# Kernel tuning notes

Hardware: AMD Instinct MI355X
Metric: run time of the kernel (lower is better)

Reference implementation:

```python
import jax, jax.numpy as jnp
import numpy as np

N_NODES = 50000

def _gat_layer(x, src, dst, W, a_l, a_r, bias, alpha, agg, act, n_nodes):
    # x: [N, in]; W: [in, H*F]; a_l, a_r: [H, F]; bias: [H*F]
    H, F = a_l.shape
    z = (x @ W).reshape(n_nodes, H, F)                      # [N,H,F]
    el = jnp.einsum('nhf,hf->nh', z, a_l)                   # [N,H]
    er = jnp.einsum('nhf,hf->nh', z, a_r)                   # [N,H]
    e = jax.nn.leaky_relu(el[src] + er[dst], alpha)         # [E,H]
    # segment softmax over in-edges of each destination node
    m = jax.ops.segment_max(e, dst, num_segments=n_nodes)   # [N,H]
    ex = jnp.exp(e - m[dst])                                # [E,H]
    s = jax.ops.segment_sum(ex, dst, num_segments=n_nodes)  # [N,H]
    attn = ex / jnp.maximum(s[dst], 1e-9)                   # [E,H]
    msg = attn[:, :, None] * z[src]                         # [E,H,F]
    h = jax.ops.segment_sum(msg, dst, num_segments=n_nodes) # [N,H,F]
    # identity residual (in_feats == H*F) as in DGL GATConv
    h = h + x.reshape(n_nodes, -1, F)
    h = h + bias.reshape(1, H, F)
    if agg == 'flatten':
        h = h.reshape(n_nodes, H * F)
    else:  # mean over heads
        h = h.mean(axis=1)
    if act is not None:
        h = act(h)
    return h


def setup_inputs() -> dict:
    key = jax.random.key(0)
    ks = jax.random.split(key, 14)
    N, E, D = N_NODES, 800000, 128
    H, F = 4, 32
    sc_in = 1.0 / np.sqrt(D)
    sc_h = 1.0 / np.sqrt(H * F)
    inp = {
        'feats': jax.random.normal(ks[0], (N, D), jnp.float32),
        'src': jax.random.randint(ks[1], (E,), 0, N),
        'dst': jax.random.randint(ks[2], (E,), 0, N),
        'W1': jax.random.normal(ks[3], (D, H * F), jnp.float32) * sc_in,
        'al1': jax.random.normal(ks[4], (H, F), jnp.float32) * sc_h,
        'ar1': jax.random.normal(ks[5], (H, F), jnp.float32) * sc_h,
        'b1': jnp.zeros((H * F,), jnp.float32),
        'W2': jax.random.normal(ks[6], (H * F, H * F), jnp.float32) * sc_h,
        'al2': jax.random.normal(ks[7], (H, F), jnp.float32) * sc_h,
        'ar2': jax.random.normal(ks[8], (H, F), jnp.float32) * sc_h,
        'b2': jnp.zeros((H * F,), jnp.float32),
        'Wp': jax.random.normal(ks[9], (F, 1), jnp.float32) / np.sqrt(F),
        'bp': jnp.zeros((1,), jnp.float32),
    }
    return inp


def reference(feats, src, dst, W1, al1, ar1, b1, W2, al2, ar2, b2, Wp, bp):
    h = _gat_layer(feats, src, dst, W1, al1, ar1, b1, 0.2, 'flatten', jax.nn.elu, N_NODES)
    h = _gat_layer(h, src, dst, W2, al2, ar2, b2, 0.2, 'mean', None, N_NODES)
    return h @ Wp + bp  # [N, 1]
```

## Files before the change

kernel.cpp:

```cpp
#include <hip/hip_runtime.h>
#include <hip/hip_bf16.h>

#define NN 50000
#define NE 800000
#define HF 128

#define OFF_FLAG   0u
#define OFF_ROWPTR 256u
#define OFF_BSUM   200272u
#define OFF_BOFF   200480u
#define OFF_DEG    200704u
#define OFF_FILL   400896u
#define OFF_ADJ    601088u
#define OFF_FX     3801088u
#define OFF_WC1    16601088u
#define OFF_WC2    16633856u
#define OFF_PAR    16666624u
#define OFF_Z      16668672u
#define OFF_H1     29468672u
#define OFF_EL     42268672u
#define OFF_ER     43068672u

typedef __hip_bfloat16 bf16;
typedef unsigned short us16;

#define N_SMALL 33569

typedef __attribute__((ext_vector_type(8))) short bf16x8;
typedef __attribute__((ext_vector_type(4))) float f32x4;

__device__ __forceinline__ float us2f(us16 u) {
  union { unsigned int i; float f; } c; c.i = ((unsigned int)u) << 16; return c.f;
}
__device__ __forceinline__ us16 f2us(float f) {
  bf16 h = __float2bfloat16(f);
  union { bf16 h; us16 u; } c; c.h = h; return c.u;
}
__device__ __forceinline__ float blo(unsigned v) {
  union { unsigned i; float f; } c; c.i = v << 16; return c.f;
}
__device__ __forceinline__ float bhi(unsigned v) {
  union { unsigned i; float f; } c; c.i = v & 0xffff0000u; return c.f;
}
__device__ __forceinline__ unsigned pk2(float a, float b) {
  return (unsigned)f2us(a) | ((unsigned)f2us(b) << 16);
}

__global__ __launch_bounds__(64) void k_detect(const void* __restrict__ w1raw,
                                               int* __restrict__ flag) {
  const us16* u = (const us16*)w1raw;
  int lane = threadIdx.x;
  int mx = 0;
  for (int i = lane; i < 2048; i += 64) {
    int e = (u[i] >> 7) & 0xFF;
    mx = mx > e ? mx : e;
  }
#pragma unroll
  for (int m = 32; m >= 1; m >>= 1) {
    int o = __shfl_xor(mx, m);
    mx = mx > o ? mx : o;
  }
  if (lane == 0) *flag = (mx >= 135) ? 1 : 0;
}

__global__ __launch_bounds__(256) void k_canon_feats(const void* __restrict__ src,
                                                     us16* __restrict__ dst,
                                                     const int* __restrict__ flag) {
  int i = (blockIdx.x * 256 + threadIdx.x) * 4;
  if (i >= NN * HF) return;
  if (*flag) {
    float4 v = *(const float4*)((const float*)src + i);
    ushort4 o;
    o.x = f2us(v.x); o.y = f2us(v.y); o.z = f2us(v.z); o.w = f2us(v.w);
    *(ushort4*)(dst + i) = o;
  } else {
    *(ushort4*)(dst + i) = *(const ushort4*)((const us16*)src + i);
  }
}

__global__ __launch_bounds__(256) void k_canon_small(
    const void* s0, const void* s1, const void* s2, const void* s3, const void* s4,
    const void* s5, const void* s6, const void* s7, const void* s8, const void* s9,
    us16* d0, us16* d1, us16* d2, us16* d3, us16* d4,
    us16* d5, us16* d6, us16* d7, us16* d8, us16* d9,
    const int* __restrict__ flag) {
  const void* sp[10] = {s0, s1, s2, s3, s4, s5, s6, s7, s8, s9};
  us16* dp[10] = {d0, d1, d2, d3, d4, d5, d6, d7, d8, d9};
  const int cnt[10] = {16384, 16384, 128, 128, 128, 128, 128, 128, 32, 1};
  int f = *flag;
  int gid = blockIdx.x * 256 + threadIdx.x;
  int base = 0;
#pragma unroll
  for (int p = 0; p < 10; ++p) {
    int loc = gid - base;
    if (loc >= 0 && loc < cnt[p])
      dp[p][loc] = f ? f2us(((const float*)sp[p])[loc]) : ((const us16*)sp[p])[loc];
    base += cnt[p];
  }
}

__global__ void k_rank(const int* __restrict__ dst, int* __restrict__ fill,
                       int* __restrict__ rank) {
  int e = blockIdx.x * 256 + threadIdx.x;
  if (e < NE) rank[e] = atomicAdd(&fill[dst[e]], 1);
}

__global__ __launch_bounds__(1024) void k_s1(const int* __restrict__ deg,
                                             int* __restrict__ bsum) {
  __shared__ int red[1024];
  int t = threadIdx.x;
  int i = blockIdx.x * 1024 + t;
  red[t] = (i < NN) ? deg[i] : 0;
  __syncthreads();
  for (int s = 512; s > 0; s >>= 1) {
    if (t < s) red[t] += red[t + s];
    __syncthreads();
  }
  if (t == 0) bsum[blockIdx.x] = red[0];
}

__global__ __launch_bounds__(64) void k_s2(const int* __restrict__ bsum,
                                           int* __restrict__ boff,
                                           int* __restrict__ rowptr) {
  int lane = threadIdx.x;
  const int NB = (NN + 1023) / 1024;
  int v = (lane < NB) ? bsum[lane] : 0;
  int orig = v;
#pragma unroll
  for (int off = 1; off < 64; off <<= 1) {
    int u = __shfl_up(v, off);
    if (lane >= off) v += u;
  }
  if (lane < NB) boff[lane] = v - orig;
  if (lane == 0) rowptr[NN] = NE;
}

__global__ __launch_bounds__(1024) void k_s3(const int* __restrict__ deg,
                                             const int* __restrict__ boff,
                                             int* __restrict__ rowptr) {
  __shared__ int part[1024];
  int t = threadIdx.x;
  int i = blockIdx.x * 1024 + t;
  int d = (i < NN) ? deg[i] : 0;
  part[t] = d;
  __syncthreads();
  for (int off = 1; off < 1024; off <<= 1) {
    int v = (t >= off) ? part[t - off] : 0;
    __syncthreads();
    part[t] += v;
    __syncthreads();
  }
  if (i < NN) rowptr[i] = boff[blockIdx.x] + part[t] - d;
}

__global__ void k_place(const int* __restrict__ src, const int* __restrict__ dst,
                        const int* __restrict__ rowptr, const int* __restrict__ rank,
                        int* __restrict__ adj) {
  int e = blockIdx.x * 256 + threadIdx.x;
  if (e < NE) adj[rowptr[dst[e]] + rank[e]] = src[e];
}

__global__ __launch_bounds__(256) void k_gemm(const us16* __restrict__ X,
                                              const us16* __restrict__ W,
                                              us16* __restrict__ Z,
                                              const us16* __restrict__ al,
                                              const us16* __restrict__ ar,
                                              float* __restrict__ el,
                                              float* __restrict__ er) {
  __shared__ us16 Wl[HF * HF];
  int tid = threadIdx.x;
  for (int e = tid; e < HF * HF; e += 256) {
    int k = e >> 7, n = e & 127;
    int d = ((((k >> 5) * 8 + (n >> 4)) * 4 + ((k >> 3) & 3)) * 16 + (n & 15)) * 8 + (k & 7);
    Wl[d] = W[e];
  }
  __syncthreads();

  int w = tid >> 6;
  int lane = tid & 63;
  int q = lane >> 4;
  int c = lane & 15;
  int m0 = blockIdx.x * 64 + w * 16;

  int rA = m0 + c;
  if (rA >= NN) rA = NN - 1;
  const us16* xrow = X + (size_t)rA * HF;

  f32x4 acc[8] = {};
#pragma unroll
  for (int s = 0; s < 4; ++s) {
    bf16x8 a = *(const bf16x8*)&xrow[s * 32 + q * 8];
#pragma unroll
    for (int t = 0; t < 8; ++t) {
      bf16x8 b = *(const bf16x8*)&Wl[((((s * 8) + t) * 4 + q) * 16 + c) * 8];
      acc[t] = __builtin_amdgcn_mfma_f32_16x16x32_bf16(a, b, acc[t], 0, 0, 0);
    }
  }

#pragma unroll
  for (int reg = 0; reg < 4; ++reg) {
    int row = m0 + q * 4 + reg;
    if (row < NN) {
      us16* zrow = Z + (size_t)row * HF;
#pragma unroll
      for (int t = 0; t < 8; ++t) zrow[t * 16 + c] = f2us(acc[t][reg]);
    }
  }

  float alv[8], arv[8];
#pragma unroll
  for (int t = 0; t < 8; ++t) {
    alv[t] = us2f(al[t * 16 + c]);
    arv[t] = us2f(ar[t * 16 + c]);
  }
#pragma unroll
  for (int reg = 0; reg < 4; ++reg) {
    int row = m0 + q * 4 + reg;
    float pl[4], pr[4];
#pragma unroll
    for (int h = 0; h < 4; ++h) {
      pl[h] = acc[2 * h][reg] * alv[2 * h] + acc[2 * h + 1][reg] * alv[2 * h + 1];
      pr[h] = acc[2 * h][reg] * arv[2 * h] + acc[2 * h + 1][reg] * arv[2 * h + 1];
    }
#pragma unroll
    for (int m = 1; m < 16; m <<= 1) {
#pragma unroll
      for (int h = 0; h < 4; ++h) {
        pl[h] += __shfl_xor(pl[h], m);
        pr[h] += __shfl_xor(pr[h], m);
      }
    }
    if (row < NN) {
      int cc = c & 3;
      float vl = cc == 0 ? pl[0] : cc == 1 ? pl[1] : cc == 2 ? pl[2] : pl[3];
      float vr = cc == 0 ? pr[0] : cc == 1 ? pr[1] : cc == 2 ? pr[2] : pr[3];
      if (c < 4) el[row * 4 + cc] = vl;
      else if (c < 8) er[row * 4 + cc] = vr;
    }
  }
}

template <int LAYER>
__global__ __launch_bounds__(256) void k_agg(
    const us16* __restrict__ Z, const float* __restrict__ el,
    const float* __restrict__ er, const int* __restrict__ rowptr,
    const int* __restrict__ adj, const us16* __restrict__ resid,
    const us16* __restrict__ bias, us16* __restrict__ Hout,
    const us16* __restrict__ Wp, const us16* __restrict__ bp,
    void* __restrict__ out, const int* __restrict__ flag) {
  int n = blockIdx.x * 4 + (threadIdx.x >> 6);
  int lane = threadIdx.x & 63;
  int g = lane >> 4;
  int p = lane & 15;
  int hl = p >> 2;
  int f0 = p * 8;
  int begin = rowptr[n];
  int deg = rowptr[n + 1] - begin;
  float erh = er[n * 4 + hl];

  float acc[8] = {};
  float ssum = 0.f;
  int i = g;
  for (; i + 4 < deg; i += 8) {
    int s0 = adj[begin + i];
    int s1 = adj[begin + i + 4];
    float l0 = el[s0 * 4 + hl];
    float l1 = el[s1 * 4 + hl];
    uint4 za = *(const uint4*)&Z[(size_t)s0 * HF + f0];
    uint4 zb = *(const uint4*)&Z[(size_t)s1 * HF + f0];
    float sc0 = l0 + erh; sc0 = sc0 > 0.f ? sc0 : 0.2f * sc0;
    float sc1 = l1 + erh; sc1 = sc1 > 0.f ? sc1 : 0.2f * sc1;
    float ex0 = __expf(sc0);
    float ex1 = __expf(sc1);
    ssum += ex0 + ex1;
    acc[0] = fmaf(ex0, blo(za.x), acc[0]); acc[1] = fmaf(ex0, bhi(za.x), acc[1]);
    acc[2] = fmaf(ex0, blo(za.y), acc[2]); acc[3] = fmaf(ex0, bhi(za.y), acc[3]);
    acc[4] = fmaf(ex0, blo(za.z), acc[4]); acc[5] = fmaf(ex0, bhi(za.z), acc[5]);
    acc[6] = fmaf(ex0, blo(za.w), acc[6]); acc[7] = fmaf(ex0, bhi(za.w), acc[7]);
    acc[0] = fmaf(ex1, blo(zb.x), acc[0]); acc[1] = fmaf(ex1, bhi(zb.x), acc[1]);
    acc[2] = fmaf(ex1, blo(zb.y), acc[2]); acc[3] = fmaf(ex1, bhi(zb.y), acc[3]);
    acc[4] = fmaf(ex1, blo(zb.z), acc[4]); acc[5] = fmaf(ex1, bhi(zb.z), acc[5]);
    acc[6] = fmaf(ex1, blo(zb.w), acc[6]); acc[7] = fmaf(ex1, bhi(zb.w), acc[7]);
  }
  if (i < deg) {
    int s = adj[begin + i];
    float sc = el[s * 4 + hl] + erh;
    sc = sc > 0.f ? sc : 0.2f * sc;
    float ex = __expf(sc);
    ssum += ex;
    uint4 zq = *(const uint4*)&Z[(size_t)s * HF + f0];
    acc[0] = fmaf(ex, blo(zq.x), acc[0]); acc[1] = fmaf(ex, bhi(zq.x), acc[1]);
    acc[2] = fmaf(ex, blo(zq.y), acc[2]); acc[3] = fmaf(ex, bhi(zq.y), acc[3]);
    acc[4] = fmaf(ex, blo(zq.z), acc[4]); acc[5] = fmaf(ex, bhi(zq.z), acc[5]);
    acc[6] = fmaf(ex, blo(zq.w), acc[6]); acc[7] = fmaf(ex, bhi(zq.w), acc[7]);
  }
  ssum += __shfl_xor(ssum, 16); ssum += __shfl_xor(ssum, 32);
#pragma unroll
  for (int j = 0; j < 8; ++j) {
    acc[j] += __shfl_xor(acc[j], 16);
    acc[j] += __shfl_xor(acc[j], 32);
  }
  float inv = 1.f / fmaxf(ssum, 1e-9f);

  uint4 xq = *(const uint4*)&resid[(size_t)n * HF + f0];
  uint4 bq = *(const uint4*)&bias[f0];
  float t0 = fmaf(acc[0], inv, blo(xq.x) + blo(bq.x));
  float t1 = fmaf(acc[1], inv, bhi(xq.x) + bhi(bq.x));
  float t2 = fmaf(acc[2], inv, blo(xq.y) + blo(bq.y));
  float t3 = fmaf(acc[3], inv, bhi(xq.y) + bhi(bq.y));
  float t4 = fmaf(acc[4], inv, blo(xq.z) + blo(bq.z));
  float t5 = fmaf(acc[5], inv, bhi(xq.z) + bhi(bq.z));
  float t6 = fmaf(acc[6], inv, blo(xq.w) + blo(bq.w));
  float t7 = fmaf(acc[7], inv, bhi(xq.w) + bhi(bq.w));

  if (LAYER == 1) {
    t0 = t0 > 0.f ? t0 : __expf(t0) - 1.f;
    t1 = t1 > 0.f ? t1 : __expf(t1) - 1.f;
    t2 = t2 > 0.f ? t2 : __expf(t2) - 1.f;
    t3 = t3 > 0.f ? t3 : __expf(t3) - 1.f;
    t4 = t4 > 0.f ? t4 : __expf(t4) - 1.f;
    t5 = t5 > 0.f ? t5 : __expf(t5) - 1.f;
    t6 = t6 > 0.f ? t6 : __expf(t6) - 1.f;
    t7 = t7 > 0.f ? t7 : __expf(t7) - 1.f;
    if (g == 0) {
      uint4 o;
      o.x = pk2(t0, t1); o.y = pk2(t2, t3); o.z = pk2(t4, t5); o.w = pk2(t6, t7);
      *(uint4*)&Hout[(size_t)n * HF + f0] = o;
    }
  } else {
    t0 += __shfl_xor(t0, 4); t0 += __shfl_xor(t0, 8);
    t1 += __shfl_xor(t1, 4); t1 += __shfl_xor(t1, 8);
    t2 += __shfl_xor(t2, 4); t2 += __shfl_xor(t2, 8);
    t3 += __shfl_xor(t3, 4); t3 += __shfl_xor(t3, 8);
    t4 += __shfl_xor(t4, 4); t4 += __shfl_xor(t4, 8);
    t5 += __shfl_xor(t5, 4); t5 += __shfl_xor(t5, 8);
    t6 += __shfl_xor(t6, 4); t6 += __shfl_xor(t6, 8);
    t7 += __shfl_xor(t7, 4); t7 += __shfl_xor(t7, 8);
    int fw = (p & 3) * 8;
    float pr = 0.25f * (t0 * us2f(Wp[fw]) + t1 * us2f(Wp[fw + 1]) +
                        t2 * us2f(Wp[fw + 2]) + t3 * us2f(Wp[fw + 3]) +
                        t4 * us2f(Wp[fw + 4]) + t5 * us2f(Wp[fw + 5]) +
                        t6 * us2f(Wp[fw + 6]) + t7 * us2f(Wp[fw + 7]));
    pr += __shfl_xor(pr, 1); pr += __shfl_xor(pr, 2);
    if (lane == 0) {
      float res = pr + us2f(bp[0]);
      if (*flag) ((float*)out)[n] = res;
      else ((us16*)out)[n] = f2us(res);
    }
  }
}

extern "C" void kernel_launch(void* const* d_in, const int* in_sizes, int n_in,
                              void* d_out, int out_size, void* d_ws, size_t ws_size,
                              hipStream_t stream) {
  const int* src = (const int*)d_in[1];
  const int* dst = (const int*)d_in[2];
  char* ws = (char*)d_ws;
  int* flag   = (int*)(ws + OFF_FLAG);
  int* rowptr = (int*)(ws + OFF_ROWPTR);
  int* bsum   = (int*)(ws + OFF_BSUM);
  int* boff   = (int*)(ws + OFF_BOFF);
  int* fill   = (int*)(ws + OFF_FILL);
  int* adj    = (int*)(ws + OFF_ADJ);
  us16* fx    = (us16*)(ws + OFF_FX);
  us16* wc1   = (us16*)(ws + OFF_WC1);
  us16* wc2   = (us16*)(ws + OFF_WC2);
  us16* al1   = (us16*)(ws + OFF_PAR + 0);
  us16* ar1   = (us16*)(ws + OFF_PAR + 256);
  us16* b1    = (us16*)(ws + OFF_PAR + 512);
  us16* al2   = (us16*)(ws + OFF_PAR + 768);
  us16* ar2   = (us16*)(ws + OFF_PAR + 1024);
  us16* b2    = (us16*)(ws + OFF_PAR + 1280);
  us16* wp    = (us16*)(ws + OFF_PAR + 1536);
  us16* bp    = (us16*)(ws + OFF_PAR + 1792);
  us16* z     = (us16*)(ws + OFF_Z);
  us16* h1    = (us16*)(ws + OFF_H1);
  float* el   = (float*)(ws + OFF_EL);
  float* er   = (float*)(ws + OFF_ER);
  int* rank   = (int*)(ws + OFF_Z);

  const int NB = (NN + 1023) / 1024;

  hipMemsetAsync(fill, 0, OFF_ADJ - OFF_FILL, stream);

  hipLaunchKernelGGL(k_detect, dim3(1), dim3(64), 0, stream, d_in[3], flag);
  hipLaunchKernelGGL(k_canon_feats, dim3(6250), dim3(256), 0, stream, d_in[0], fx, flag);
  hipLaunchKernelGGL(k_canon_small, dim3((N_SMALL + 255) / 256), dim3(256), 0, stream,
                     d_in[3], d_in[7], d_in[4], d_in[5], d_in[6],
                     d_in[8], d_in[9], d_in[10], d_in[11], d_in[12],
                     wc1, wc2, al1, ar1, b1, al2, ar2, b2, wp, bp, flag);

  hipLaunchKernelGGL(k_rank, dim3(3125), dim3(256), 0, stream, dst, fill, rank);
  hipLaunchKernelGGL(k_s1, dim3(NB), dim3(1024), 0, stream, fill, bsum);
  hipLaunchKernelGGL(k_s2, dim3(1), dim3(64), 0, stream, bsum, boff, rowptr);
  hipLaunchKernelGGL(k_s3, dim3(NB), dim3(1024), 0, stream, fill, boff, rowptr);
  hipLaunchKernelGGL(k_place, dim3(3125), dim3(256), 0, stream, src, dst, rowptr, rank, adj);

  hipLaunchKernelGGL(k_gemm, dim3((NN + 63) / 64), dim3(256), 0, stream, fx, wc1, z,
                     al1, ar1, el, er);
  hipLaunchKernelGGL((k_agg<1>), dim3(NN / 4), dim3(256), 0, stream, z, el, er, rowptr, adj,
                     fx, b1, h1, (us16*)nullptr, (us16*)nullptr, (void*)nullptr, flag);
  hipLaunchKernelGGL(k_gemm, dim3((NN + 63) / 64), dim3(256), 0, stream, h1, wc2, z,
                     al2, ar2, el, er);
  hipLaunchKernelGGL((k_agg<2>), dim3(NN / 4), dim3(256), 0, stream, z, el, er, rowptr, adj,
                     h1, b2, (us16*)nullptr, wp, bp, d_out, flag);
}
```

Measured before the change: 264.0 us.

## Fuse detect, canonicalize and edge-rank kernels into one prep launch with padded counters

Merges the dtype detection, feature and parameter canonicalization, and the atomic in-degree ranking into a single kernel whose block ranges do different jobs. Each block recomputes the dtype flag locally, so no separate detect launch is needed. The per-node atomic counters are spread 64 bytes apart to reduce atomic contention, and they now live in the H1 buffer. This cuts four launches to one and lets the atomics overlap the conversion work, at the cost of a larger memset, redundant detection reads in every conversion block, and strided counter reads in the scans.

Result: faster. 254.5 us (-3.6%).

```diff
diff --git a/kernel.cpp b/kernel.cpp
--- a/kernel.cpp
+++ b/kernel.cpp
@@ -26,6 +26,11 @@
 
 #define N_SMALL 33569
 
+#define PREP_RANK_B   3125
+#define PREP_FEATS_B  6250
+#define PREP_SMALL_B  132
+#define PREP_GRID     (PREP_RANK_B + PREP_FEATS_B + PREP_SMALL_B)
+
 typedef __attribute__((ext_vector_type(8))) short bf16x8;
 typedef __attribute__((ext_vector_type(4))) float f32x4;
 
@@ -46,12 +51,10 @@
   return (unsigned)f2us(a) | ((unsigned)f2us(b) << 16);
 }
 
-__global__ __launch_bounds__(64) void k_detect(const void* __restrict__ w1raw,
-                                               int* __restrict__ flag) {
-  const us16* u = (const us16*)w1raw;
-  int lane = threadIdx.x;
+__device__ __forceinline__ int detect_f32(const us16* __restrict__ u) {
+  int t = threadIdx.x;
   int mx = 0;
-  for (int i = lane; i < 2048; i += 64) {
+  for (int i = t; i < 2048; i += 256) {
     int e = (u[i] >> 7) & 0xFF;
     mx = mx > e ? mx : e;
   }
@@ -60,57 +63,63 @@
     int o = __shfl_xor(mx, m);
     mx = mx > o ? mx : o;
   }
-  if (lane == 0) *flag = (mx >= 135) ? 1 : 0;
-}
-
-__global__ __launch_bounds__(256) void k_canon_feats(const void* __restrict__ src,
-                                                     us16* __restrict__ dst,
-                                                     const int* __restrict__ flag) {
-  int i = (blockIdx.x * 256 + threadIdx.x) * 4;
-  if (i >= NN * HF) return;
-  if (*flag) {
-    float4 v = *(const float4*)((const float*)src + i);
-    ushort4 o;
-    o.x = f2us(v.x); o.y = f2us(v.y); o.z = f2us(v.z); o.w = f2us(v.w);
-    *(ushort4*)(dst + i) = o;
-  } else {
-    *(ushort4*)(dst + i) = *(const ushort4*)((const us16*)src + i);
-  }
-}
-
-__global__ __launch_bounds__(256) void k_canon_small(
+  __shared__ int sred[4];
+  if ((t & 63) == 0) sred[t >> 6] = mx;
+  __syncthreads();
+  int a = sred[0] > sred[1] ? sred[0] : sred[1];
+  int b = sred[2] > sred[3] ? sred[2] : sred[3];
+  int r = a > b ? a : b;
+  return r >= 135;
+}
+
+__global__ __launch_bounds__(256) void k_prep(
+    const void* __restrict__ feats, us16* __restrict__ fx,
     const void* s0, const void* s1, const void* s2, const void* s3, const void* s4,
     const void* s5, const void* s6, const void* s7, const void* s8, const void* s9,
     us16* d0, us16* d1, us16* d2, us16* d3, us16* d4,
     us16* d5, us16* d6, us16* d7, us16* d8, us16* d9,
-    const int* __restrict__ flag) {
-  const void* sp[10] = {s0, s1, s2, s3, s4, s5, s6, s7, s8, s9};
-  us16* dp[10] = {d0, d1, d2, d3, d4, d5, d6, d7, d8, d9};
-  const int cnt[10] = {16384, 16384, 128, 128, 128, 128, 128, 128, 32, 1};
-  int f = *flag;
-  int gid = blockIdx.x * 256 + threadIdx.x;
-  int base = 0;
-#pragma unroll
-  for (int p = 0; p < 10; ++p) {
-    int loc = gid - base;
-    if (loc >= 0 && loc < cnt[p])
-      dp[p][loc] = f ? f2us(((const float*)sp[p])[loc]) : ((const us16*)sp[p])[loc];
-    base += cnt[p];
-  }
-}
-
-__global__ void k_rank(const int* __restrict__ dst, int* __restrict__ fill,
-                       int* __restrict__ rank) {
-  int e = blockIdx.x * 256 + threadIdx.x;
-  if (e < NE) rank[e] = atomicAdd(&fill[dst[e]], 1);
-}
-
-__global__ __launch_bounds__(1024) void k_s1(const int* __restrict__ deg,
+    const int* __restrict__ dst, int* __restrict__ fillp, int* __restrict__ rank,
+    int* __restrict__ flag) {
+  int b = blockIdx.x;
+  if (b < PREP_RANK_B) {
+    int e = b * 256 + threadIdx.x;
+    if (e < NE) rank[e] = atomicAdd(&fillp[dst[e] * 16], 1);
+    return;
+  }
+  int f = detect_f32((const us16*)s0);
+  if (b == PREP_RANK_B && threadIdx.x == 0) *flag = f;
+  if (b < PREP_RANK_B + PREP_FEATS_B) {
+    int i = ((b - PREP_RANK_B) * 256 + threadIdx.x) * 4;
+    if (f) {
+      float4 v = *(const float4*)((const float*)feats + i);
+      ushort4 o;
+      o.x = f2us(v.x); o.y = f2us(v.y); o.z = f2us(v.z); o.w = f2us(v.w);
+      *(ushort4*)(fx + i) = o;
+    } else {
+      *(ushort4*)(fx + i) = *(const ushort4*)((const us16*)feats + i);
+    }
+  } else {
+    const void* sp[10] = {s0, s1, s2, s3, s4, s5, s6, s7, s8, s9};
+    us16* dp[10] = {d0, d1, d2, d3, d4, d5, d6, d7, d8, d9};
+    const int cnt[10] = {16384, 16384, 128, 128, 128, 128, 128, 128, 32, 1};
+    int gid = (b - PREP_RANK_B - PREP_FEATS_B) * 256 + threadIdx.x;
+    int base = 0;
+#pragma unroll
+    for (int p = 0; p < 10; ++p) {
+      int loc = gid - base;
+      if (loc >= 0 && loc < cnt[p])
+        dp[p][loc] = f ? f2us(((const float*)sp[p])[loc]) : ((const us16*)sp[p])[loc];
+      base += cnt[p];
+    }
+  }
+}
+
+__global__ __launch_bounds__(1024) void k_s1(const int* __restrict__ fillp,
                                              int* __restrict__ bsum) {
   __shared__ int red[1024];
   int t = threadIdx.x;
   int i = blockIdx.x * 1024 + t;
-  red[t] = (i < NN) ? deg[i] : 0;
+  red[t] = (i < NN) ? fillp[i * 16] : 0;
   __syncthreads();
   for (int s = 512; s > 0; s >>= 1) {
     if (t < s) red[t] += red[t + s];
@@ -135,13 +144,13 @@
   if (lane == 0) rowptr[NN] = NE;
 }
 
-__global__ __launch_bounds__(1024) void k_s3(const int* __restrict__ deg,
+__global__ __launch_bounds__(1024) void k_s3(const int* __restrict__ fillp,
                                              const int* __restrict__ boff,
                                              int* __restrict__ rowptr) {
   __shared__ int part[1024];
   int t = threadIdx.x;
   int i = blockIdx.x * 1024 + t;
-  int d = (i < NN) ? deg[i] : 0;
+  int d = (i < NN) ? fillp[i * 16] : 0;
   part[t] = d;
   __syncthreads();
   for (int off = 1; off < 1024; off <<= 1) {
@@ -360,7 +369,6 @@
   int* rowptr = (int*)(ws + OFF_ROWPTR);
   int* bsum   = (int*)(ws + OFF_BSUM);
   int* boff   = (int*)(ws + OFF_BOFF);
-  int* fill   = (int*)(ws + OFF_FILL);
   int* adj    = (int*)(ws + OFF_ADJ);
   us16* fx    = (us16*)(ws + OFF_FX);
   us16* wc1   = (us16*)(ws + OFF_WC1);
@@ -378,22 +386,22 @@
   float* el   = (float*)(ws + OFF_EL);
   float* er   = (float*)(ws + OFF_ER);
   int* rank   = (int*)(ws + OFF_Z);
+  int* fillp  = (int*)(ws + OFF_H1);
 
   const int NB = (NN + 1023) / 1024;
 
-  hipMemsetAsync(fill, 0, OFF_ADJ - OFF_FILL, stream);
-
-  hipLaunchKernelGGL(k_detect, dim3(1), dim3(64), 0, stream, d_in[3], flag);
-  hipLaunchKernelGGL(k_canon_feats, dim3(6250), dim3(256), 0, stream, d_in[0], fx, flag);
-  hipLaunchKernelGGL(k_canon_small, dim3((N_SMALL + 255) / 256), dim3(256), 0, stream,
+  hipMemsetAsync(fillp, 0, (size_t)NN * 16 * 4, stream);
+
+  hipLaunchKernelGGL(k_prep, dim3(PREP_GRID), dim3(256), 0, stream,
+                     d_in[0], fx,
                      d_in[3], d_in[7], d_in[4], d_in[5], d_in[6],
                      d_in[8], d_in[9], d_in[10], d_in[11], d_in[12],
-                     wc1, wc2, al1, ar1, b1, al2, ar2, b2, wp, bp, flag);
-
-  hipLaunchKernelGGL(k_rank, dim3(3125), dim3(256), 0, stream, dst, fill, rank);
-  hipLaunchKernelGGL(k_s1, dim3(NB), dim3(1024), 0, stream, fill, bsum);
+                     wc1, wc2, al1, ar1, b1, al2, ar2, b2, wp, bp,
+                     dst, fillp, rank, flag);
+
+  hipLaunchKernelGGL(k_s1, dim3(NB), dim3(1024), 0, stream, fillp, bsum);
   hipLaunchKernelGGL(k_s2, dim3(1), dim3(64), 0, stream, bsum, boff, rowptr);
-  hipLaunchKernelGGL(k_s3, dim3(NB), dim3(1024), 0, stream, fill, boff, rowptr);
+  hipLaunchKernelGGL(k_s3, dim3(NB), dim3(1024), 0, stream, fillp, boff, rowptr);
   hipLaunchKernelGGL(k_place, dim3(3125), dim3(256), 0, stream, src, dst, rowptr, rank, adj);
 
   hipLaunchKernelGGL(k_gemm, dim3((NN + 63) / 64), dim3(256), 0, stream, fx, wc1, z,
```
